# Kernel tuning notes

Hardware: AMD Instinct MI355X
Metric: run time of the kernel (lower is better)

Reference implementation:

```python
import jax, jax.numpy as jnp
import numpy as np

VOC, TOPIC, EMB, BATCH = 128000, 512, 1024, 1024

def setup_inputs() -> dict:
    key = jax.random.key(0)
    k1, k2, k3 = jax.random.split(key, 3)
    x = jax.random.normal(k1, (TOPIC, BATCH), dtype=jnp.float32)
    beta0 = jax.random.normal(k2, (VOC, EMB), dtype=jnp.float32)
    beta_t = jax.random.normal(k3, (TOPIC, EMB), dtype=jnp.float32) * 0.02  # nn.init.normal_(std=0.02)
    return {"x": x, "beta0": beta0, "beta_t": beta_t, "t": 0}

def reference(x, beta0, beta_t, t):
    # w: [voc, topic] = beta0 [voc, emb] @ beta_t.T [emb, topic]
    # (the t==0 branch and else branch are identical in the source)
    w = jnp.einsum('ve,te->vt', beta0, beta_t)
    w = jax.nn.softmax(w, axis=0)  # softmax over vocab dim (dim=0)
    # out: [voc, batch]
    return jnp.einsum('vt,tb->vb', w, x)
```

## Files before the change

kernel.cpp:

```cpp
#include <hip/hip_runtime.h>

typedef _Float16 f16x8 __attribute__((ext_vector_type(8)));
typedef float    f32x4 __attribute__((ext_vector_type(4)));
typedef unsigned short u16;

#define VOC   128000
#define TOPIC 512
#define EMB   1024
#define BATCH 1024

__device__ __forceinline__ int swz32(int row, int kbyte) {
    return row * 64 + (kbyte ^ (((row >> 1) & 3) << 4));
}
__device__ __forceinline__ int xcd_swz(int bid, int nwg) {
    int x = bid & 7, o = bid >> 3, q = nwg >> 3, r = nwg & 7;
    return (x < r ? x * (q + 1) : r * (q + 1) + (x - r) * q) + o;
}
union H2U { _Float16 h; u16 u; };

#define SBAR() asm volatile("s_barrier" ::: "memory")
#define WVM0() asm volatile("s_waitcnt vmcnt(0)" ::: "memory")
#define WVM4() asm volatile("s_waitcnt vmcnt(4)" ::: "memory")
#define WVM8() asm volatile("s_waitcnt vmcnt(8)" ::: "memory")
#define WLG0() asm volatile("s_waitcnt lgkmcnt(0)" ::: "memory")

#define GLDS(SRC, DST) __builtin_amdgcn_global_load_lds( \
    (const __attribute__((address_space(1))) unsigned int*)(SRC), \
    (__attribute__((address_space(3))) unsigned int*)(DST), 16, 0, 0)

#define RD_A(BUF, MH) { _Pragma("unroll") \
    for (int m = 0; m < 4; ++m) \
        af[m] = *(const f16x8*)((BUF) + swz32(wr * 128 + (MH) * 64 + m * 16 + lr, lk * 16)); }
#define RD_B(BUF) { _Pragma("unroll") \
    for (int n = 0; n < 4; ++n) \
        bf[n] = *(const f16x8*)((BUF) + 16384 + swz32(wc * 64 + n * 16 + lr, lk * 16)); }
#define MFMA16(MH) { \
    __builtin_amdgcn_s_setprio(1); \
    _Pragma("unroll") for (int m = 0; m < 4; ++m) \
    _Pragma("unroll") for (int n = 0; n < 4; ++n) \
        acc[(MH) * 4 + m][n] = __builtin_amdgcn_mfma_f32_16x16x32_f16( \
            af[m], bf[n], acc[(MH) * 4 + m][n], 0, 0, 0); \
    __builtin_amdgcn_s_setprio(0); }

__global__ void cvt_betat_kernel(const float* __restrict__ betat, u16* __restrict__ bt16) {
    const size_t g = (size_t)blockIdx.x * 256 + threadIdx.x;
    const float4* src = reinterpret_cast<const float4*>(betat) + g * 2;
    float4 a = src[0], b = src[1];
    f16x8 h;
    h[0]=(_Float16)a.x; h[1]=(_Float16)a.y; h[2]=(_Float16)a.z; h[3]=(_Float16)a.w;
    h[4]=(_Float16)b.x; h[5]=(_Float16)b.y; h[6]=(_Float16)b.z; h[7]=(_Float16)b.w;
    *(reinterpret_cast<f16x8*>(bt16) + g) = h;
}

__global__ __launch_bounds__(512, 2) void gemm1_kernel(
    const float* __restrict__ beta0, const u16* __restrict__ bt16,
    u16* __restrict__ Eg, float* __restrict__ sg)
{
    __shared__ char lds[131072];

    const int tid  = threadIdx.x;
    const int lane = tid & 63;
    const int wid  = tid >> 6;
    const int wr = wid >> 2, wc = wid & 3;
    const int lr = lane & 15, lk = lane >> 4;
    const int srcRow   = lane >> 2;
    const int srcChunk = (lane & 3) ^ ((lane >> 3) & 3);

    const int bid   = xcd_swz(blockIdx.x, gridDim.x);
    const int tile  = bid >> 1;
    const int chunk = bid & 1;
    const int v0 = tile * 256, t0 = chunk * 256;

    const int arow = tid >> 1, ahalf = tid & 1;
    const float* aBase = beta0 + (size_t)(v0 + arow) * EMB + ahalf * 16;

    f32x4 acc[8][4] = {};
    f16x8 af[4], bf[4];
    float4 rEv[4], rOd[4];

#define G1_LOADA(R, KT) { const float4* gp = (const float4*)(aBase + (KT) * 32); \
    R[0] = gp[0]; R[1] = gp[1]; R[2] = gp[2]; R[3] = gp[3]; }
#define G1_CVT(R, KT1) { char* dA = lds + ((KT1) & 3) * 32768; \
    f16x8 h0, h1; \
    h0[0]=(_Float16)R[0].x; h0[1]=(_Float16)R[0].y; h0[2]=(_Float16)R[0].z; h0[3]=(_Float16)R[0].w; \
    h0[4]=(_Float16)R[1].x; h0[5]=(_Float16)R[1].y; h0[6]=(_Float16)R[1].z; h0[7]=(_Float16)R[1].w; \
    h1[0]=(_Float16)R[2].x; h1[1]=(_Float16)R[2].y; h1[2]=(_Float16)R[2].z; h1[3]=(_Float16)R[2].w; \
    h1[4]=(_Float16)R[3].x; h1[5]=(_Float16)R[3].y; h1[6]=(_Float16)R[3].z; h1[7]=(_Float16)R[3].w; \
    *(f16x8*)(dA + swz32(arow, (ahalf * 2) * 16)) = h0; \
    *(f16x8*)(dA + swz32(arow, (ahalf * 2 + 1) * 16)) = h1; }

    auto stageB_ = [&](int kt) {
        char* dst = lds + (kt & 3) * 32768 + 16384;
        const u16* s0 = bt16 + (size_t)(t0 + wid * 32 + srcRow) * EMB + kt * 32 + srcChunk * 8;
        GLDS(s0, dst + wid * 32 * 64);
        GLDS(s0 + (size_t)16 * EMB, dst + (wid * 32 + 16) * 64);
    };

    stageB_(0);
    G1_LOADA(rEv, 0);
    stageB_(1); stageB_(2);
    G1_LOADA(rOd, 1);
    G1_CVT(rEv, 0);
    WLG0();

#define G1_TILE(T, RC, RI) { \
    WVM8(); SBAR(); \
    char* buf = lds + ((T) & 3) * 32768; \
    RD_A(buf, 0); RD_B(buf); \
    if ((T) + 2 < 32) G1_LOADA(RI, (T) + 2); \
    MFMA16(0); \
    SBAR(); \
    RD_A(buf, 1); \
    if ((T) + 1 < 32) G1_CVT(RC, (T) + 1); \
    if ((T) + 3 < 32) stageB_((T) + 3); \
    MFMA16(1); \
    WLG0(); }

    for (int tt = 0; tt < 16; ++tt) {
        const int t = tt * 2;
        G1_TILE(t,     rOd, rEv);
        G1_TILE(t + 1, rEv, rOd);
    }

    __syncthreads();
    u16* ldsE = reinterpret_cast<u16*>(lds);
    float csum = 0.f;
    #pragma unroll
    for (int c = 0; c < 4; ++c) {
        if (wr == (c >> 1)) {
            const int mb = (c & 1) * 4;
            #pragma unroll
            for (int m = 0; m < 4; ++m)
              #pragma unroll
              for (int n = 0; n < 4; ++n)
                #pragma unroll
                for (int r = 0; r < 4; ++r) {
                    const int row = m * 16 + lk * 4 + r;
                    const int col = wc * 64 + n * 16 + lr;
                    H2U cv; cv.h = (_Float16)__expf(acc[mb + m][n][r]);
                    ldsE[row * 264 + col] = cv.u;
                }
        }
        __syncthreads();
        {
            const int row8 = tid >> 3, seg = tid & 7;
            const int4* sp = reinterpret_cast<const int4*>(&ldsE[row8 * 264 + seg * 32]);
            u16* dst = Eg + (size_t)(v0 + c * 64 + row8) * 2048 + t0 + seg * 32;
            int4 a0 = sp[0], a1 = sp[1], a2 = sp[2], a3 = sp[3];
            int4* dp = reinterpret_cast<int4*>(dst);
            dp[0] = a0; dp[1] = a1; dp[2] = a2; dp[3] = a3;
        }
        if (tid < 256) {
            float s = 0.f;
            for (int r = 0; r < 64; ++r) { H2U cv; cv.u = ldsE[r * 264 + tid]; s += (float)cv.h; }
            csum += s;
        }
        __syncthreads();
    }
    if (tid < 256) atomicAdd(sg + t0 + tid, csum);
}

__global__ void xst_kernel(const float* __restrict__ x, const float* __restrict__ s,
                           u16* __restrict__ xsT)
{
    __shared__ float tile[32][33];
    const int b0 = blockIdx.x * 32, t0 = blockIdx.y * 32;
    const int tx = threadIdx.x, ty = threadIdx.y;
    tile[ty][tx] = x[(size_t)(t0 + ty) * BATCH + b0 + tx];
    __syncthreads();
    const float sc = 65536.0f / s[t0 + tx];
    H2U cv; cv.h = (_Float16)(tile[tx][ty] * sc);
    xsT[(size_t)(b0 + ty) * TOPIC + t0 + tx] = cv.u;
}

__global__ __launch_bounds__(512, 2) void gemm2_kernel(
    const u16* __restrict__ Eg, const u16* __restrict__ xsT,
    float* __restrict__ out, int c0, int nch)
{
    __shared__ char lds[131072];

    const int tid  = threadIdx.x;
    const int lane = tid & 63;
    const int wid  = tid >> 6;
    const int wr = wid >> 2, wc = wid & 3;
    const int lr = lane & 15, lk = lane >> 4;
    const int srcRow   = lane >> 2;
    const int srcChunk = (lane & 3) ^ ((lane >> 3) & 3);

    const int bid   = xcd_swz(blockIdx.x, gridDim.x);
    const int tile  = bid / nch;
    const int chunk = bid % nch;
    const int v0 = tile * 256, b0 = (c0 + chunk) * 256;

    f32x4 acc[8][4] = {};
    f16x8 af[4], bf[4];

    auto stageA_ = [&](int kt) {
        char* dst = lds + (kt & 3) * 32768;
        const u16* s0 = Eg + (size_t)(v0 + wid * 32 + srcRow) * 2048 + kt * 32 + srcChunk * 8;
        GLDS(s0, dst + wid * 32 * 64);
        GLDS(s0 + (size_t)16 * 2048, dst + (wid * 32 + 16) * 64);
    };
    auto stageB_ = [&](int kt) {
        char* dst = lds + (kt & 3) * 32768 + 16384;
        const u16* s0 = xsT + (size_t)(b0 + wid * 32 + srcRow) * TOPIC + kt * 32 + srcChunk * 8;
        GLDS(s0, dst + wid * 32 * 64);
        GLDS(s0 + (size_t)16 * TOPIC, dst + (wid * 32 + 16) * 64);
    };

    stageA_(0); stageB_(0); stageA_(1); stageB_(1); stageA_(2); stageB_(2);

    for (int t = 0; t < 16; ++t) {
        if (t <= 13) { WVM8(); } else if (t == 14) { WVM4(); } else { WVM0(); }
        SBAR();
        char* buf = lds + (t & 3) * 32768;
        RD_A(buf, 0); RD_B(buf);
        if (t + 3 < 16) stageA_(t + 3);
        MFMA16(0);
        SBAR();
        RD_A(buf, 1);
        if (t + 3 < 16) stageB_(t + 3);
        MFMA16(1);
    }

    #pragma unroll
    for (int mh = 0; mh < 2; ++mh)
      #pragma unroll
      for (int m = 0; m < 4; ++m)
        #pragma unroll
        for (int n = 0; n < 4; ++n)
          #pragma unroll
          for (int r = 0; r < 4; ++r) {
              const int row = wr * 128 + mh * 64 + m * 16 + lk * 4 + r;
              const int col = wc * 64 + n * 16 + lr;
              out[(size_t)(v0 + row) * BATCH + b0 + col] = acc[mh * 4 + m][n][r] * 0x1p-16f;
          }
}

extern "C" void kernel_launch(void* const* d_in, const int* in_sizes, int n_in,
                              void* d_out, int out_size, void* d_ws, size_t ws_size,
                              hipStream_t stream)
{
    const float* x     = (const float*)d_in[0];
    const float* beta0 = (const float*)d_in[1];
    const float* betat = (const float*)d_in[2];
    float* out = (float*)d_out;

    const size_t need_min = 4096 + (size_t)BATCH * TOPIC * 2;
    if (ws_size < need_min) return;
    float* s_g  = (float*)d_ws;
    u16*   buf1 = (u16*)((char*)d_ws + 4096);

    hipMemsetAsync(d_ws, 0, 2048, stream);
    cvt_betat_kernel<<<256, 256, 0, stream>>>(betat, buf1);

    u16* EgO = (u16*)d_out;
    gemm1_kernel<<<1000, 512, 0, stream>>>(beta0, buf1, EgO, s_g);

    xst_kernel<<<dim3(BATCH / 32, TOPIC / 32), dim3(32, 32), 0, stream>>>(x, s_g, buf1);

    gemm2_kernel<<<1500, 512, 0, stream>>>(EgO, buf1, out, 1, 3);
    gemm2_kernel<<<500,  512, 0, stream>>>(EgO, buf1, out, 0, 1);
}
```

Baseline: 506.7 us.

## Shrink LDS ring to three stages and drop mid-tile barrier in both GEMMs

Both GEMM kernels move from a 4-deep LDS ring with prefetch distance 3 to a 3-deep ring with prefetch distance 2, shrinking shared memory from 128 KiB to 96 KiB. The second s_barrier inside each K-step is removed. In gemm1 the order of B staging, A register loads and the fp16 conversion into LDS is rearranged, and the explicit vmcnt wait is dropped. The aim is to cut synchronisation overhead per tile. The risk is less latency hiding with the shallower prefetch, plus subtle ordering hazards now that completion of the async LDS loads is only implied by waits on register loads.

After: 512.4 us. No clear change (+1.1%).

```diff
diff --git a/kernel.cpp b/kernel.cpp
--- a/kernel.cpp
+++ b/kernel.cpp
@@ -21,7 +21,6 @@
 #define SBAR() asm volatile("s_barrier" ::: "memory")
 #define WVM0() asm volatile("s_waitcnt vmcnt(0)" ::: "memory")
 #define WVM4() asm volatile("s_waitcnt vmcnt(4)" ::: "memory")
-#define WVM8() asm volatile("s_waitcnt vmcnt(8)" ::: "memory")
 #define WLG0() asm volatile("s_waitcnt lgkmcnt(0)" ::: "memory")
 
 #define GLDS(SRC, DST) __builtin_amdgcn_global_load_lds( \
@@ -52,11 +51,11 @@
     *(reinterpret_cast<f16x8*>(bt16) + g) = h;
 }
 
-__global__ __launch_bounds__(512, 2) void gemm1_kernel(
+__global__ __launch_bounds__(512) void gemm1_kernel(
     const float* __restrict__ beta0, const u16* __restrict__ bt16,
     u16* __restrict__ Eg, float* __restrict__ sg)
 {
-    __shared__ char lds[131072];
+    __shared__ char lds[98304];
 
     const int tid  = threadIdx.x;
     const int lane = tid & 63;
@@ -80,17 +79,17 @@
 
 #define G1_LOADA(R, KT) { const float4* gp = (const float4*)(aBase + (KT) * 32); \
     R[0] = gp[0]; R[1] = gp[1]; R[2] = gp[2]; R[3] = gp[3]; }
-#define G1_CVT(R, KT1) { char* dA = lds + ((KT1) & 3) * 32768; \
+#define G1_CVT(R, KT1) { char* dA = lds + ((KT1) % 3) * 32768; \
     f16x8 h0, h1; \
     h0[0]=(_Float16)R[0].x; h0[1]=(_Float16)R[0].y; h0[2]=(_Float16)R[0].z; h0[3]=(_Float16)R[0].w; \
     h0[4]=(_Float16)R[1].x; h0[5]=(_Float16)R[1].y; h0[6]=(_Float16)R[1].z; h0[7]=(_Float16)R[1].w; \
     h1[0]=(_Float16)R[2].x; h1[1]=(_Float16)R[2].y; h1[2]=(_Float16)R[2].z; h1[3]=(_Float16)R[2].w; \
     h1[4]=(_Float16)R[3].x; h1[5]=(_Float16)R[3].y; h1[6]=(_Float16)R[3].z; h1[7]=(_Float16)R[3].w; \
-    *(f16x8*)(dA + swz32(arow, (ahalf * 2) * 16)) = h0; \
-    *(f16x8*)(dA + swz32(arow, (ahalf * 2 + 1) * 16)) = h1; }
+    *(f16x8*)(dA + swz32(arow, ahalf * 32 + 0))  = h0; \
+    *(f16x8*)(dA + swz32(arow, ahalf * 32 + 16)) = h1; }
 
     auto stageB_ = [&](int kt) {
-        char* dst = lds + (kt & 3) * 32768 + 16384;
+        char* dst = lds + (kt % 3) * 32768 + 16384;
         const u16* s0 = bt16 + (size_t)(t0 + wid * 32 + srcRow) * EMB + kt * 32 + srcChunk * 8;
         GLDS(s0, dst + wid * 32 * 64);
         GLDS(s0 + (size_t)16 * EMB, dst + (wid * 32 + 16) * 64);
@@ -98,22 +97,21 @@
 
     stageB_(0);
     G1_LOADA(rEv, 0);
-    stageB_(1); stageB_(2);
-    G1_LOADA(rOd, 1);
     G1_CVT(rEv, 0);
     WLG0();
+    stageB_(1);
+    G1_LOADA(rOd, 1);
 
 #define G1_TILE(T, RC, RI) { \
-    WVM8(); SBAR(); \
-    char* buf = lds + ((T) & 3) * 32768; \
+    SBAR(); \
+    char* buf = lds + ((T) % 3) * 32768; \
     RD_A(buf, 0); RD_B(buf); \
+    if ((T) + 2 < 32) stageB_((T) + 2); \
+    MFMA16(0); \
+    RD_A(buf, 1); \
     if ((T) + 2 < 32) G1_LOADA(RI, (T) + 2); \
-    MFMA16(0); \
-    SBAR(); \
-    RD_A(buf, 1); \
-    if ((T) + 1 < 32) G1_CVT(RC, (T) + 1); \
-    if ((T) + 3 < 32) stageB_((T) + 3); \
     MFMA16(1); \
+    if ((T) + 1 < 32) { G1_CVT(RC, (T) + 1); } \
     WLG0(); }
 
     for (int tt = 0; tt < 16; ++tt) {
@@ -173,11 +171,11 @@
     xsT[(size_t)(b0 + ty) * TOPIC + t0 + tx] = cv.u;
 }
 
-__global__ __launch_bounds__(512, 2) void gemm2_kernel(
+__global__ __launch_bounds__(512) void gemm2_kernel(
     const u16* __restrict__ Eg, const u16* __restrict__ xsT,
     float* __restrict__ out, int c0, int nch)
 {
-    __shared__ char lds[131072];
+    __shared__ char lds[98304];
 
     const int tid  = threadIdx.x;
     const int lane = tid & 63;
@@ -196,30 +194,30 @@
     f16x8 af[4], bf[4];
 
     auto stageA_ = [&](int kt) {
-        char* dst = lds + (kt & 3) * 32768;
+        char* dst = lds + (kt % 3) * 32768;
         const u16* s0 = Eg + (size_t)(v0 + wid * 32 + srcRow) * 2048 + kt * 32 + srcChunk * 8;
         GLDS(s0, dst + wid * 32 * 64);
         GLDS(s0 + (size_t)16 * 2048, dst + (wid * 32 + 16) * 64);
     };
     auto stageB_ = [&](int kt) {
-        char* dst = lds + (kt & 3) * 32768 + 16384;
+        char* dst = lds + (kt % 3) * 32768 + 16384;
         const u16* s0 = xsT + (size_t)(b0 + wid * 32 + srcRow) * TOPIC + kt * 32 + srcChunk * 8;
         GLDS(s0, dst + wid * 32 * 64);
         GLDS(s0 + (size_t)16 * TOPIC, dst + (wid * 32 + 16) * 64);
     };
 
-    stageA_(0); stageB_(0); stageA_(1); stageB_(1); stageA_(2); stageB_(2);
+    stageA_(0); stageB_(0);
+    stageA_(1); stageB_(1);
 
     for (int t = 0; t < 16; ++t) {
-        if (t <= 13) { WVM8(); } else if (t == 14) { WVM4(); } else { WVM0(); }
+        if (t < 15) { WVM4(); } else { WVM0(); }
         SBAR();
-        char* buf = lds + (t & 3) * 32768;
+        char* buf = lds + (t % 3) * 32768;
         RD_A(buf, 0); RD_B(buf);
-        if (t + 3 < 16) stageA_(t + 3);
+        if (t + 2 < 16) stageA_(t + 2);
         MFMA16(0);
-        SBAR();
         RD_A(buf, 1);
-        if (t + 3 < 16) stageB_(t + 3);
+        if (t + 2 < 16) stageB_(t + 2);
         MFMA16(1);
     }
 
```
